# Performance work log

Hardware: AMD Instinct MI355X
Metric: run time of the kernel (lower is better)

## Reference

```python
import jax, jax.numpy as jnp
import numpy as np

EPS = 1e-12


def setup_inputs() -> dict:
    key = jax.random.key(0)
    k1, k2, k3, k4 = jax.random.split(key, 4)
    N, H, W, D, K = 64, 32, 32, 512, 64
    x = jax.random.normal(k1, (N, H, W, D), dtype=jnp.float32)
    W_assign = jax.random.normal(k2, (D, K), dtype=jnp.float32) * 0.05  # 1x1 conv kernel
    b_assign = jax.random.normal(k3, (K,), dtype=jnp.float32) * 0.05
    C = jax.random.normal(k4, (D, K), dtype=jnp.float32) * 0.05  # cluster centers
    return {"x": x, "W_assign": W_assign, "b_assign": b_assign, "C": C}


def _l2norm(v, axis):
    return v / jnp.sqrt(jnp.sum(v * v, axis=axis, keepdims=True) + EPS)


def reference(x, W_assign, b_assign, C):
    # 1x1 conv = matmul over channel dim: [N,H,W,D] @ [D,K] -> [N,H,W,K]
    s = jnp.einsum('nhwd,dk->nhwk', x, W_assign) + b_assign
    a = jax.nn.softmax(s, axis=-1)                       # soft assignment over K
    # VLAD: v[n,d,k] = sum_hw a[n,h,w,k] * (x[n,h,w,d] + C[d,k])
    # reformulated as two small contractions (no [N,H,W,D,K] intermediate):
    v = jnp.einsum('nhwd,nhwk->ndk', x, a)               # feature-weighted sums
    a_sum = jnp.sum(a, axis=(1, 2))                      # [N,K]
    v = v + a_sum[:, None, :] * C[None, :, :]            # [N,D,K]
    # intra-normalization: L2 over D per cluster (after transpose to [N,K,D])
    v = _l2norm(jnp.transpose(v, (0, 2, 1)), axis=-1)    # [N,K,D]
    v = jnp.transpose(v, (0, 2, 1))                      # [N,D,K]
    # flatten and final L2 normalize -> [N, D*K]
    v = v.reshape(v.shape[0], -1)
    return _l2norm(v, axis=-1)
```

## Files before the change

kernel.cpp:

```cpp
#include <hip/hip_runtime.h>


#define EPSF 1e-12f

typedef short bf16x8 __attribute__((ext_vector_type(8)));
typedef float f32x16 __attribute__((ext_vector_type(16)));

__device__ inline unsigned short f2bf_rne(float f) {
  union { float f; unsigned u; } v; v.f = f;
  unsigned u = v.u;
  unsigned r = u + 0x7fffu + ((u >> 16) & 1u);
  return (unsigned short)(r >> 16);
}
__device__ inline float bf2f(unsigned short h) {
  union { unsigned u; float f; } v; v.u = ((unsigned)h) << 16;
  return v.f;
}

__global__ __launch_bounds__(256) void kprep(
    const float* __restrict__ Wm,
    unsigned short* __restrict__ wt_hi, unsigned short* __restrict__ wt_lo) {
  __shared__ float tile[64][65];
  const int t = threadIdx.x, bx = blockIdx.x;
  {
    int col = (t & 15) * 4, rbase = t >> 4;
#pragma unroll
    for (int r = 0; r < 4; ++r) {
      int row = rbase + 16 * r;
      *(float4*)&tile[row][col] =
          *(const float4*)&Wm[(size_t)(bx * 64 + row) * 64 + col];
    }
  }
  __syncthreads();
  int k = t >> 2, seg = (t & 3) * 16;
  size_t o = (size_t)k * 512 + bx * 64 + seg;
#pragma unroll
  for (int j = 0; j < 16; j += 2) {
    float f0 = tile[seg + j][k], f1 = tile[seg + j + 1][k];
    unsigned short h0 = f2bf_rne(f0), h1 = f2bf_rne(f1);
    unsigned short l0 = f2bf_rne(f0 - bf2f(h0)), l1 = f2bf_rne(f1 - bf2f(h1));
    *(unsigned*)&wt_hi[o + j] = (unsigned)h0 | ((unsigned)h1 << 16);
    *(unsigned*)&wt_lo[o + j] = (unsigned)l0 | ((unsigned)l1 << 16);
  }
}

__global__ __launch_bounds__(256) void kassign(
    const float* __restrict__ x,
    const unsigned short* __restrict__ wt_hi,
    const unsigned short* __restrict__ wt_lo,
    const float* __restrict__ b,
    unsigned short* __restrict__ at_hi, unsigned short* __restrict__ at_lo,
    float* __restrict__ a_sum) {
  __shared__ unsigned short xs_hi[128][72];
  __shared__ unsigned short xs_lo[128][72];
  __shared__ unsigned short ws_hi[64][72];
  __shared__ unsigned short ws_lo[64][72];
  const int t = threadIdx.x;
  const int w = t >> 6, lane = t & 63, l31 = lane & 31, h = lane >> 5;
  const int p0 = blockIdx.x * 128;

  f32x16 acc0, acc1;
#pragma unroll
  for (int i = 0; i < 16; ++i) { acc0[i] = 0.f; acc1[i] = 0.f; }

  for (int c = 0; c < 8; ++c) {
    const int dc = c * 64;
    __syncthreads();
    {
      int col = (t & 15) * 4, rbase = t >> 4;
#pragma unroll
      for (int r = 0; r < 8; ++r) {
        int row = rbase + 16 * r;
        float4 xv = *(const float4*)&x[(size_t)(p0 + row) * 512 + dc + col];
        unsigned short h0 = f2bf_rne(xv.x), h1 = f2bf_rne(xv.y);
        unsigned short h2 = f2bf_rne(xv.z), h3 = f2bf_rne(xv.w);
        unsigned short l0 = f2bf_rne(xv.x - bf2f(h0)), l1 = f2bf_rne(xv.y - bf2f(h1));
        unsigned short l2 = f2bf_rne(xv.z - bf2f(h2)), l3 = f2bf_rne(xv.w - bf2f(h3));
        uint2 ph, pl;
        ph.x = (unsigned)h0 | ((unsigned)h1 << 16); ph.y = (unsigned)h2 | ((unsigned)h3 << 16);
        pl.x = (unsigned)l0 | ((unsigned)l1 << 16); pl.y = (unsigned)l2 | ((unsigned)l3 << 16);
        *(uint2*)&xs_hi[row][col] = ph;
        *(uint2*)&xs_lo[row][col] = pl;
      }
    }
    {
      int k = t >> 2, seg = (t & 3) * 16;
      size_t g = (size_t)k * 512 + dc + seg;
      *(uint4*)&ws_hi[k][seg] = *(const uint4*)&wt_hi[g];
      *(uint4*)&ws_hi[k][seg + 8] = *(const uint4*)&wt_hi[g + 8];
      *(uint4*)&ws_lo[k][seg] = *(const uint4*)&wt_lo[g];
      *(uint4*)&ws_lo[k][seg + 8] = *(const uint4*)&wt_lo[g + 8];
    }
    __syncthreads();
#pragma unroll
    for (int s = 0; s < 4; ++s) {
      int kd = s * 16 + h * 8;
      bf16x8 axh = *(const bf16x8*)&xs_hi[32 * w + l31][kd];
      bf16x8 axl = *(const bf16x8*)&xs_lo[32 * w + l31][kd];
      bf16x8 b0h = *(const bf16x8*)&ws_hi[l31][kd];
      bf16x8 b0l = *(const bf16x8*)&ws_lo[l31][kd];
      bf16x8 b1h = *(const bf16x8*)&ws_hi[32 + l31][kd];
      bf16x8 b1l = *(const bf16x8*)&ws_lo[32 + l31][kd];
      acc0 = __builtin_amdgcn_mfma_f32_32x32x16_bf16(axh, b0h, acc0, 0, 0, 0);
      acc0 = __builtin_amdgcn_mfma_f32_32x32x16_bf16(axl, b0h, acc0, 0, 0, 0);
      acc0 = __builtin_amdgcn_mfma_f32_32x32x16_bf16(axh, b0l, acc0, 0, 0, 0);
      acc1 = __builtin_amdgcn_mfma_f32_32x32x16_bf16(axh, b1h, acc1, 0, 0, 0);
      acc1 = __builtin_amdgcn_mfma_f32_32x32x16_bf16(axl, b1h, acc1, 0, 0, 0);
      acc1 = __builtin_amdgcn_mfma_f32_32x32x16_bf16(axh, b1l, acc1, 0, 0, 0);
    }
  }

  const float bias0 = b[l31], bias1 = b[32 + l31];
  float a0[16], a1[16];
  float sum0 = 0.f, sum1 = 0.f;
#pragma unroll
  for (int r = 0; r < 16; ++r) {
    float s0 = acc0[r] + bias0, s1 = acc1[r] + bias1;
    float m = fmaxf(s0, s1);
#pragma unroll
    for (int msk = 1; msk < 32; msk <<= 1) m = fmaxf(m, __shfl_xor(m, msk, 64));
    float e0 = __expf(s0 - m), e1 = __expf(s1 - m);
    float S = e0 + e1;
#pragma unroll
    for (int msk = 1; msk < 32; msk <<= 1) S += __shfl_xor(S, msk, 64);
    float inv = 1.0f / S;
    a0[r] = e0 * inv; a1[r] = e1 * inv;
    sum0 += a0[r]; sum1 += a1[r];
  }
  const int n = p0 >> 10;
  const int hwb = (p0 & 1023) + 32 * w + 4 * h;
  const size_t kb0 = ((size_t)n * 64 + l31) * 1024;
  const size_t kb1 = ((size_t)n * 64 + 32 + l31) * 1024;
#pragma unroll
  for (int g = 0; g < 4; ++g) {
    int hw = hwb + 8 * g;
    unsigned short vh[8], vl[8];
#pragma unroll
    for (int j = 0; j < 4; ++j) {
      unsigned short hh = f2bf_rne(a0[4 * g + j]);
      vh[j] = hh; vl[j] = f2bf_rne(a0[4 * g + j] - bf2f(hh));
      unsigned short hh1 = f2bf_rne(a1[4 * g + j]);
      vh[4 + j] = hh1; vl[4 + j] = f2bf_rne(a1[4 * g + j] - bf2f(hh1));
    }
    uint2 u;
    u.x = (unsigned)vh[0] | ((unsigned)vh[1] << 16); u.y = (unsigned)vh[2] | ((unsigned)vh[3] << 16);
    *(uint2*)&at_hi[kb0 + hw] = u;
    u.x = (unsigned)vl[0] | ((unsigned)vl[1] << 16); u.y = (unsigned)vl[2] | ((unsigned)vl[3] << 16);
    *(uint2*)&at_lo[kb0 + hw] = u;
    u.x = (unsigned)vh[4] | ((unsigned)vh[5] << 16); u.y = (unsigned)vh[6] | ((unsigned)vh[7] << 16);
    *(uint2*)&at_hi[kb1 + hw] = u;
    u.x = (unsigned)vl[4] | ((unsigned)vl[5] << 16); u.y = (unsigned)vl[6] | ((unsigned)vl[7] << 16);
    *(uint2*)&at_lo[kb1 + hw] = u;
  }
  sum0 += __shfl_xor(sum0, 32, 64);
  sum1 += __shfl_xor(sum1, 32, 64);
  if (lane < 32) {
    atomicAdd(&a_sum[n * 64 + l31], sum0);
    atomicAdd(&a_sum[n * 64 + 32 + l31], sum1);
  }
}

__global__ __launch_bounds__(256) void kvlad(
    const float* __restrict__ x,
    const unsigned short* __restrict__ at_hi,
    const unsigned short* __restrict__ at_lo,
    const float* __restrict__ a_sum, const float* __restrict__ C,
    float* __restrict__ out) {
  __shared__ float xs[64][68];
  __shared__ unsigned short ash[64][72];
  __shared__ unsigned short asl[64][72];
  const int t = threadIdx.x;
  const int w = t >> 6, lane = t & 63, l31 = lane & 31, h = lane >> 5;
  const int n = blockIdx.y, d0 = blockIdx.x * 64;
  const int dw = 32 * (w & 1);
  const int kw = 32 * (w >> 1);
  const float* xb = x + (size_t)n * 1024 * 512;

  f32x16 acc;
#pragma unroll
  for (int i = 0; i < 16; ++i) acc[i] = 0.f;

  for (int c = 0; c < 16; ++c) {
    const int hw0 = c * 64;
    __syncthreads();
    {
      int col = (t & 15) * 4, rbase = t >> 4;
#pragma unroll
      for (int r = 0; r < 4; ++r) {
        int row = rbase + 16 * r;
        *(float4*)&xs[row][col] =
            *(const float4*)&xb[(size_t)(hw0 + row) * 512 + d0 + col];
      }
    }
    {
      int k = t >> 2, seg = (t & 3) * 16;
      size_t g = ((size_t)n * 64 + k) * 1024 + hw0 + seg;
      *(uint4*)&ash[k][seg] = *(const uint4*)&at_hi[g];
      *(uint4*)&ash[k][seg + 8] = *(const uint4*)&at_hi[g + 8];
      *(uint4*)&asl[k][seg] = *(const uint4*)&at_lo[g];
      *(uint4*)&asl[k][seg + 8] = *(const uint4*)&at_lo[g + 8];
    }
    __syncthreads();
#pragma unroll
    for (int s = 0; s < 4; ++s) {
      int kk = s * 16 + h * 8;
      bf16x8 axh, axl;
#pragma unroll
      for (int j = 0; j < 8; ++j) {
        float f = xs[kk + j][dw + l31];
        unsigned short hi = f2bf_rne(f);
        axh[j] = (short)hi;
        axl[j] = (short)f2bf_rne(f - bf2f(hi));
      }
      bf16x8 bh = *(const bf16x8*)&ash[kw + l31][kk];
      bf16x8 bl = *(const bf16x8*)&asl[kw + l31][kk];
      acc = __builtin_amdgcn_mfma_f32_32x32x16_bf16(axh, bh, acc, 0, 0, 0);
      acc = __builtin_amdgcn_mfma_f32_32x32x16_bf16(axl, bh, acc, 0, 0, 0);
      acc = __builtin_amdgcn_mfma_f32_32x32x16_bf16(axh, bl, acc, 0, 0, 0);
    }
  }
  const float as = a_sum[n * 64 + kw + l31];
#pragma unroll
  for (int r = 0; r < 16; ++r) {
    int row = (r & 3) + 8 * (r >> 2) + 4 * h;
    int d = d0 + dw + row;
    float cv = C[(size_t)d * 64 + kw + l31];
    out[((size_t)n * 512 + d) * 64 + kw + l31] = acc[r] + as * cv;
  }
}

__global__ __launch_bounds__(256) void kssq(
    const float* __restrict__ out, float* __restrict__ ssq) {
  const int n = blockIdx.y, slice = blockIdx.x;
  const int t = threadIdx.x, k = t & 63, rg = t >> 6;
  const float* vb = out + (size_t)n * 32768 + (size_t)slice * 4096;
  float s = 0.f;
#pragma unroll
  for (int r = rg; r < 64; r += 4) { float v = vb[r * 64 + k]; s += v * v; }
  __shared__ float red[64];
  if (t < 64) red[t] = 0.f;
  __syncthreads();
  atomicAdd(&red[k], s);
  __syncthreads();
  if (t < 64) atomicAdd(&ssq[n * 64 + t], red[t]);
}

__global__ __launch_bounds__(256) void kscale(
    float* __restrict__ out, const float* __restrict__ ssq) {
  const int n = blockIdx.y, slice = blockIdx.x;
  const int t = threadIdx.x, k = t & 63, rg = t >> 6;
  __shared__ float sk[64];
  __shared__ float tot;
  if (t < 64) {
    float c = ssq[n * 64 + t];
    sk[t] = rsqrtf(c + EPSF);
    float contrib = c / (c + EPSF);
#pragma unroll
    for (int m = 32; m; m >>= 1) contrib += __shfl_xor(contrib, m, 64);
    if (t == 0) tot = rsqrtf(contrib + EPSF);
  }
  __syncthreads();
  const float scale = sk[k] * tot;
  float* vb = out + (size_t)n * 32768 + (size_t)slice * 4096;
#pragma unroll
  for (int r = rg; r < 64; r += 4) vb[r * 64 + k] *= scale;
}

extern "C" void kernel_launch(void* const* d_in, const int* in_sizes, int n_in,
                              void* d_out, int out_size, void* d_ws, size_t ws_size,
                              hipStream_t stream) {
  const float* x  = (const float*)d_in[0];
  const float* Wm = (const float*)d_in[1];
  const float* b  = (const float*)d_in[2];
  const float* C  = (const float*)d_in[3];
  float* out = (float*)d_out;

  unsigned short* at_hi = (unsigned short*)d_ws;
  unsigned short* at_lo = at_hi + (size_t)64 * 64 * 1024;
  unsigned short* wt_hi = at_lo + (size_t)64 * 64 * 1024;
  unsigned short* wt_lo = wt_hi + (size_t)64 * 512;
  float* a_sum = (float*)(wt_lo + (size_t)64 * 512);
  float* ssq   = a_sum + 4096;

  hipMemsetAsync(a_sum, 0, 8192 * sizeof(float), stream);
  kprep<<<dim3(8), dim3(256), 0, stream>>>(Wm, wt_hi, wt_lo);
  kassign<<<dim3(512), dim3(256), 0, stream>>>(x, wt_hi, wt_lo, b, at_hi, at_lo, a_sum);
  kvlad<<<dim3(8, 64), dim3(256), 0, stream>>>(x, at_hi, at_lo, a_sum, C, out);
  kssq<<<dim3(8, 64), dim3(256), 0, stream>>>(out, ssq);
  kscale<<<dim3(8, 64), dim3(256), 0, stream>>>(out, ssq);
}
```

Baseline: 278.1 us.

## Drop split-bf16 precision, prefetch tiles into registers, fuse ssq into VLAD kernel

```diff
diff --git a/kernel.cpp b/kernel.cpp
--- a/kernel.cpp
+++ b/kernel.cpp
@@ -12,14 +12,12 @@
   unsigned r = u + 0x7fffu + ((u >> 16) & 1u);
   return (unsigned short)(r >> 16);
 }
-__device__ inline float bf2f(unsigned short h) {
-  union { unsigned u; float f; } v; v.u = ((unsigned)h) << 16;
-  return v.f;
+__device__ inline unsigned pk2(float a, float b) {
+  return (unsigned)f2bf_rne(a) | ((unsigned)f2bf_rne(b) << 16);
 }
 
 __global__ __launch_bounds__(256) void kprep(
-    const float* __restrict__ Wm,
-    unsigned short* __restrict__ wt_hi, unsigned short* __restrict__ wt_lo) {
+    const float* __restrict__ Wm, unsigned short* __restrict__ wt) {
   __shared__ float tile[64][65];
   const int t = threadIdx.x, bx = blockIdx.x;
   {
@@ -35,78 +33,62 @@
   int k = t >> 2, seg = (t & 3) * 16;
   size_t o = (size_t)k * 512 + bx * 64 + seg;
 #pragma unroll
-  for (int j = 0; j < 16; j += 2) {
-    float f0 = tile[seg + j][k], f1 = tile[seg + j + 1][k];
-    unsigned short h0 = f2bf_rne(f0), h1 = f2bf_rne(f1);
-    unsigned short l0 = f2bf_rne(f0 - bf2f(h0)), l1 = f2bf_rne(f1 - bf2f(h1));
-    *(unsigned*)&wt_hi[o + j] = (unsigned)h0 | ((unsigned)h1 << 16);
-    *(unsigned*)&wt_lo[o + j] = (unsigned)l0 | ((unsigned)l1 << 16);
-  }
+  for (int j = 0; j < 16; j += 2)
+    *(unsigned*)&wt[o + j] = pk2(tile[seg + j][k], tile[seg + j + 1][k]);
 }
 
 __global__ __launch_bounds__(256) void kassign(
-    const float* __restrict__ x,
-    const unsigned short* __restrict__ wt_hi,
-    const unsigned short* __restrict__ wt_lo,
-    const float* __restrict__ b,
-    unsigned short* __restrict__ at_hi, unsigned short* __restrict__ at_lo,
+    const float* __restrict__ x, const unsigned short* __restrict__ wt,
+    const float* __restrict__ b, unsigned short* __restrict__ at,
     float* __restrict__ a_sum) {
-  __shared__ unsigned short xs_hi[128][72];
-  __shared__ unsigned short xs_lo[128][72];
-  __shared__ unsigned short ws_hi[64][72];
-  __shared__ unsigned short ws_lo[64][72];
+  __shared__ unsigned short xs[128][72];
+  __shared__ unsigned short ws[64][72];
   const int t = threadIdx.x;
   const int w = t >> 6, lane = t & 63, l31 = lane & 31, h = lane >> 5;
   const int p0 = blockIdx.x * 128;
+  const int col = (t & 15) * 4, rbase = t >> 4;
+  const int wk = t >> 2, wseg = (t & 3) * 16;
+
+  float4 px[8];
+  uint4 pw0, pw1;
+#pragma unroll
+  for (int r = 0; r < 8; ++r)
+    px[r] = *(const float4*)&x[(size_t)(p0 + rbase + 16 * r) * 512 + col];
+  pw0 = *(const uint4*)&wt[(size_t)wk * 512 + wseg];
+  pw1 = *(const uint4*)&wt[(size_t)wk * 512 + wseg + 8];
 
   f32x16 acc0, acc1;
 #pragma unroll
   for (int i = 0; i < 16; ++i) { acc0[i] = 0.f; acc1[i] = 0.f; }
 
   for (int c = 0; c < 8; ++c) {
-    const int dc = c * 64;
-    __syncthreads();
-    {
-      int col = (t & 15) * 4, rbase = t >> 4;
-#pragma unroll
-      for (int r = 0; r < 8; ++r) {
-        int row = rbase + 16 * r;
-        float4 xv = *(const float4*)&x[(size_t)(p0 + row) * 512 + dc + col];
-        unsigned short h0 = f2bf_rne(xv.x), h1 = f2bf_rne(xv.y);
-        unsigned short h2 = f2bf_rne(xv.z), h3 = f2bf_rne(xv.w);
-        unsigned short l0 = f2bf_rne(xv.x - bf2f(h0)), l1 = f2bf_rne(xv.y - bf2f(h1));
-        unsigned short l2 = f2bf_rne(xv.z - bf2f(h2)), l3 = f2bf_rne(xv.w - bf2f(h3));
-        uint2 ph, pl;
-        ph.x = (unsigned)h0 | ((unsigned)h1 << 16); ph.y = (unsigned)h2 | ((unsigned)h3 << 16);
-        pl.x = (unsigned)l0 | ((unsigned)l1 << 16); pl.y = (unsigned)l2 | ((unsigned)l3 << 16);
-        *(uint2*)&xs_hi[row][col] = ph;
-        *(uint2*)&xs_lo[row][col] = pl;
-      }
-    }
-    {
-      int k = t >> 2, seg = (t & 3) * 16;
-      size_t g = (size_t)k * 512 + dc + seg;
-      *(uint4*)&ws_hi[k][seg] = *(const uint4*)&wt_hi[g];
-      *(uint4*)&ws_hi[k][seg + 8] = *(const uint4*)&wt_hi[g + 8];
-      *(uint4*)&ws_lo[k][seg] = *(const uint4*)&wt_lo[g];
-      *(uint4*)&ws_lo[k][seg + 8] = *(const uint4*)&wt_lo[g + 8];
-    }
-    __syncthreads();
+    __syncthreads();
+#pragma unroll
+    for (int r = 0; r < 8; ++r) {
+      uint2 ph;
+      ph.x = pk2(px[r].x, px[r].y);
+      ph.y = pk2(px[r].z, px[r].w);
+      *(uint2*)&xs[rbase + 16 * r][col] = ph;
+    }
+    *(uint4*)&ws[wk][wseg] = pw0;
+    *(uint4*)&ws[wk][wseg + 8] = pw1;
+    __syncthreads();
+    if (c < 7) {
+      const int dc = (c + 1) * 64;
+#pragma unroll
+      for (int r = 0; r < 8; ++r)
+        px[r] = *(const float4*)&x[(size_t)(p0 + rbase + 16 * r) * 512 + dc + col];
+      pw0 = *(const uint4*)&wt[(size_t)wk * 512 + dc + wseg];
+      pw1 = *(const uint4*)&wt[(size_t)wk * 512 + dc + wseg + 8];
+    }
 #pragma unroll
     for (int s = 0; s < 4; ++s) {
       int kd = s * 16 + h * 8;
-      bf16x8 axh = *(const bf16x8*)&xs_hi[32 * w + l31][kd];
-      bf16x8 axl = *(const bf16x8*)&xs_lo[32 * w + l31][kd];
-      bf16x8 b0h = *(const bf16x8*)&ws_hi[l31][kd];
-      bf16x8 b0l = *(const bf16x8*)&ws_lo[l31][kd];
-      bf16x8 b1h = *(const bf16x8*)&ws_hi[32 + l31][kd];
-      bf16x8 b1l = *(const bf16x8*)&ws_lo[32 + l31][kd];
-      acc0 = __builtin_amdgcn_mfma_f32_32x32x16_bf16(axh, b0h, acc0, 0, 0, 0);
-      acc0 = __builtin_amdgcn_mfma_f32_32x32x16_bf16(axl, b0h, acc0, 0, 0, 0);
-      acc0 = __builtin_amdgcn_mfma_f32_32x32x16_bf16(axh, b0l, acc0, 0, 0, 0);
-      acc1 = __builtin_amdgcn_mfma_f32_32x32x16_bf16(axh, b1h, acc1, 0, 0, 0);
-      acc1 = __builtin_amdgcn_mfma_f32_32x32x16_bf16(axl, b1h, acc1, 0, 0, 0);
-      acc1 = __builtin_amdgcn_mfma_f32_32x32x16_bf16(axh, b1l, acc1, 0, 0, 0);
+      bf16x8 ax = *(const bf16x8*)&xs[32 * w + l31][kd];
+      bf16x8 b0 = *(const bf16x8*)&ws[l31][kd];
+      bf16x8 b1 = *(const bf16x8*)&ws[32 + l31][kd];
+      acc0 = __builtin_amdgcn_mfma_f32_32x32x16_bf16(ax, b0, acc0, 0, 0, 0);
+      acc1 = __builtin_amdgcn_mfma_f32_32x32x16_bf16(ax, b1, acc1, 0, 0, 0);
     }
   }
 
@@ -134,23 +116,13 @@
 #pragma unroll
   for (int g = 0; g < 4; ++g) {
     int hw = hwb + 8 * g;
-    unsigned short vh[8], vl[8];
-#pragma unroll
-    for (int j = 0; j < 4; ++j) {
-      unsigned short hh = f2bf_rne(a0[4 * g + j]);
-      vh[j] = hh; vl[j] = f2bf_rne(a0[4 * g + j] - bf2f(hh));
-      unsigned short hh1 = f2bf_rne(a1[4 * g + j]);
-      vh[4 + j] = hh1; vl[4 + j] = f2bf_rne(a1[4 * g + j] - bf2f(hh1));
-    }
     uint2 u;
-    u.x = (unsigned)vh[0] | ((unsigned)vh[1] << 16); u.y = (unsigned)vh[2] | ((unsigned)vh[3] << 16);
-    *(uint2*)&at_hi[kb0 + hw] = u;
-    u.x = (unsigned)vl[0] | ((unsigned)vl[1] << 16); u.y = (unsigned)vl[2] | ((unsigned)vl[3] << 16);
-    *(uint2*)&at_lo[kb0 + hw] = u;
-    u.x = (unsigned)vh[4] | ((unsigned)vh[5] << 16); u.y = (unsigned)vh[6] | ((unsigned)vh[7] << 16);
-    *(uint2*)&at_hi[kb1 + hw] = u;
-    u.x = (unsigned)vl[4] | ((unsigned)vl[5] << 16); u.y = (unsigned)vl[6] | ((unsigned)vl[7] << 16);
-    *(uint2*)&at_lo[kb1 + hw] = u;
+    u.x = pk2(a0[4 * g + 0], a0[4 * g + 1]);
+    u.y = pk2(a0[4 * g + 2], a0[4 * g + 3]);
+    *(uint2*)&at[kb0 + hw] = u;
+    u.x = pk2(a1[4 * g + 0], a1[4 * g + 1]);
+    u.y = pk2(a1[4 * g + 2], a1[4 * g + 3]);
+    *(uint2*)&at[kb1 + hw] = u;
   }
   sum0 += __shfl_xor(sum0, 32, 64);
   sum1 += __shfl_xor(sum1, 32, 64);
@@ -161,88 +133,72 @@
 }
 
 __global__ __launch_bounds__(256) void kvlad(
-    const float* __restrict__ x,
-    const unsigned short* __restrict__ at_hi,
-    const unsigned short* __restrict__ at_lo,
+    const float* __restrict__ x, const unsigned short* __restrict__ at,
     const float* __restrict__ a_sum, const float* __restrict__ C,
-    float* __restrict__ out) {
+    float* __restrict__ out, float* __restrict__ ssq) {
   __shared__ float xs[64][68];
-  __shared__ unsigned short ash[64][72];
-  __shared__ unsigned short asl[64][72];
+  __shared__ unsigned short as_[64][72];
   const int t = threadIdx.x;
   const int w = t >> 6, lane = t & 63, l31 = lane & 31, h = lane >> 5;
   const int n = blockIdx.y, d0 = blockIdx.x * 64;
-  const int dw = 32 * (w & 1);
-  const int kw = 32 * (w >> 1);
+  const int dw = 32 * (w & 1), kw = 32 * (w >> 1);
   const float* xb = x + (size_t)n * 1024 * 512;
+  const int col = (t & 15) * 4, rbase = t >> 4;
+  const int ak = t >> 2, aseg = (t & 3) * 16;
+  const size_t abase = ((size_t)n * 64 + ak) * 1024;
+
+  float4 px[4];
+  uint4 pa0, pa1;
+#pragma unroll
+  for (int r = 0; r < 4; ++r)
+    px[r] = *(const float4*)&xb[(size_t)(rbase + 16 * r) * 512 + d0 + col];
+  pa0 = *(const uint4*)&at[abase + aseg];
+  pa1 = *(const uint4*)&at[abase + aseg + 8];
 
   f32x16 acc;
 #pragma unroll
   for (int i = 0; i < 16; ++i) acc[i] = 0.f;
 
   for (int c = 0; c < 16; ++c) {
-    const int hw0 = c * 64;
-    __syncthreads();
-    {
-      int col = (t & 15) * 4, rbase = t >> 4;
-#pragma unroll
-      for (int r = 0; r < 4; ++r) {
-        int row = rbase + 16 * r;
-        *(float4*)&xs[row][col] =
-            *(const float4*)&xb[(size_t)(hw0 + row) * 512 + d0 + col];
-      }
-    }
-    {
-      int k = t >> 2, seg = (t & 3) * 16;
-      size_t g = ((size_t)n * 64 + k) * 1024 + hw0 + seg;
-      *(uint4*)&ash[k][seg] = *(const uint4*)&at_hi[g];
-      *(uint4*)&ash[k][seg + 8] = *(const uint4*)&at_hi[g + 8];
-      *(uint4*)&asl[k][seg] = *(const uint4*)&at_lo[g];
-      *(uint4*)&asl[k][seg + 8] = *(const uint4*)&at_lo[g + 8];
-    }
-    __syncthreads();
+    __syncthreads();
+#pragma unroll
+    for (int r = 0; r < 4; ++r)
+      *(float4*)&xs[rbase + 16 * r][col] = px[r];
+    *(uint4*)&as_[ak][aseg] = pa0;
+    *(uint4*)&as_[ak][aseg + 8] = pa1;
+    __syncthreads();
+    if (c < 15) {
+      const int hw0 = (c + 1) * 64;
+#pragma unroll
+      for (int r = 0; r < 4; ++r)
+        px[r] = *(const float4*)&xb[(size_t)(hw0 + rbase + 16 * r) * 512 + d0 + col];
+      pa0 = *(const uint4*)&at[abase + hw0 + aseg];
+      pa1 = *(const uint4*)&at[abase + hw0 + aseg + 8];
+    }
 #pragma unroll
     for (int s = 0; s < 4; ++s) {
       int kk = s * 16 + h * 8;
-      bf16x8 axh, axl;
-#pragma unroll
-      for (int j = 0; j < 8; ++j) {
-        float f = xs[kk + j][dw + l31];
-        unsigned short hi = f2bf_rne(f);
-        axh[j] = (short)hi;
-        axl[j] = (short)f2bf_rne(f - bf2f(hi));
-      }
-      bf16x8 bh = *(const bf16x8*)&ash[kw + l31][kk];
-      bf16x8 bl = *(const bf16x8*)&asl[kw + l31][kk];
-      acc = __builtin_amdgcn_mfma_f32_32x32x16_bf16(axh, bh, acc, 0, 0, 0);
-      acc = __builtin_amdgcn_mfma_f32_32x32x16_bf16(axl, bh, acc, 0, 0, 0);
-      acc = __builtin_amdgcn_mfma_f32_32x32x16_bf16(axh, bl, acc, 0, 0, 0);
-    }
-  }
-  const float as = a_sum[n * 64 + kw + l31];
+      bf16x8 ax;
+#pragma unroll
+      for (int j = 0; j < 8; ++j)
+        ax[j] = (short)f2bf_rne(xs[kk + j][dw + l31]);
+      bf16x8 bh = *(const bf16x8*)&as_[kw + l31][kk];
+      acc = __builtin_amdgcn_mfma_f32_32x32x16_bf16(ax, bh, acc, 0, 0, 0);
+    }
+  }
+
+  const int k = kw + l31;
+  const float as = a_sum[n * 64 + k];
+  float sq = 0.f;
 #pragma unroll
   for (int r = 0; r < 16; ++r) {
     int row = (r & 3) + 8 * (r >> 2) + 4 * h;
     int d = d0 + dw + row;
-    float cv = C[(size_t)d * 64 + kw + l31];
-    out[((size_t)n * 512 + d) * 64 + kw + l31] = acc[r] + as * cv;
-  }
-}
-
-__global__ __launch_bounds__(256) void kssq(
-    const float* __restrict__ out, float* __restrict__ ssq) {
-  const int n = blockIdx.y, slice = blockIdx.x;
-  const int t = threadIdx.x, k = t & 63, rg = t >> 6;
-  const float* vb = out + (size_t)n * 32768 + (size_t)slice * 4096;
-  float s = 0.f;
-#pragma unroll
-  for (int r = rg; r < 64; r += 4) { float v = vb[r * 64 + k]; s += v * v; }
-  __shared__ float red[64];
-  if (t < 64) red[t] = 0.f;
-  __syncthreads();
-  atomicAdd(&red[k], s);
-  __syncthreads();
-  if (t < 64) atomicAdd(&ssq[n * 64 + t], red[t]);
+    float o = acc[r] + as * C[(size_t)d * 64 + k];
+    out[((size_t)n * 512 + d) * 64 + k] = o;
+    sq += o * o;
+  }
+  atomicAdd(&ssq[n * 64 + k], sq);
 }
 
 __global__ __launch_bounds__(256) void kscale(
@@ -275,17 +231,14 @@
   const float* C  = (const float*)d_in[3];
   float* out = (float*)d_out;
 
-  unsigned short* at_hi = (unsigned short*)d_ws;
-  unsigned short* at_lo = at_hi + (size_t)64 * 64 * 1024;
-  unsigned short* wt_hi = at_lo + (size_t)64 * 64 * 1024;
-  unsigned short* wt_lo = wt_hi + (size_t)64 * 512;
-  float* a_sum = (float*)(wt_lo + (size_t)64 * 512);
+  unsigned short* at = (unsigned short*)d_ws;
+  unsigned short* wt = at + (size_t)64 * 64 * 1024;
+  float* a_sum = (float*)(wt + (size_t)64 * 512);
   float* ssq   = a_sum + 4096;
 
   hipMemsetAsync(a_sum, 0, 8192 * sizeof(float), stream);
-  kprep<<<dim3(8), dim3(256), 0, stream>>>(Wm, wt_hi, wt_lo);
-  kassign<<<dim3(512), dim3(256), 0, stream>>>(x, wt_hi, wt_lo, b, at_hi, at_lo, a_sum);
-  kvlad<<<dim3(8, 64), dim3(256), 0, stream>>>(x, at_hi, at_lo, a_sum, C, out);
-  kssq<<<dim3(8, 64), dim3(256), 0, stream>>>(out, ssq);
+  kprep<<<dim3(8), dim3(256), 0, stream>>>(Wm, wt);
+  kassign<<<dim3(512), dim3(256), 0, stream>>>(x, wt, b, at, a_sum);
+  kvlad<<<dim3(8, 64), dim3(256), 0, stream>>>(x, at, a_sum, C, out, ssq);
   kscale<<<dim3(8, 64), dim3(256), 0, stream>>>(out, ssq);
 }
```

Result: no change. 274.4 us (-1.3%).
